# Kernel optimization log

Measured on AMD Instinct MI355X. Metric: run time of the kernel, lower is better.

Reference implementation:

```python
import jax, jax.numpy as jnp
import numpy as np

B, IN_CH, OUT_CH, N_SINCS, COND = 8, 2, 4, 4, 32
K, HOP, T = 256, 64, 65536
FB = K // 2 + 1
EPS = 1e-6


def _windows():
    n = jnp.arange(K, dtype=jnp.float32)
    ola = 0.5 * (1.0 - jnp.cos(2.0 * jnp.pi * n / K))                      # periodic hann
    fir = 0.42 - 0.5 * jnp.cos(2.0 * jnp.pi * n / K) + 0.08 * jnp.cos(4.0 * jnp.pi * n / K)  # periodic blackman
    return ola, fir


def _sinc(x):
    # normalized sinc matching torch.sinc / jnp.sinc, grad-safe near 0
    px = jnp.pi * x
    small = jnp.abs(px) < 1e-4
    px_safe = jnp.where(small, 1.0, px)
    return jnp.where(small, 1.0 - px * px / 6.0, jnp.sin(px_safe) / px_safe)


def _conv1d(x, w, stride, pad):
    return jax.lax.conv_general_dilated(x, w, (stride,), [(pad, pad)],
                                        dimension_numbers=('NCH', 'OIH', 'NCH'))


def setup_inputs() -> dict:
    key = jax.random.key(0)
    ks = jax.random.split(key, 7)
    return {
        'x': jax.random.normal(ks[0], (B, IN_CH, T), jnp.float32),
        'conditioning': jax.random.normal(ks[1], (B, COND, T), jnp.float32),
        'w1': 0.02 * jax.random.normal(ks[2], (COND, COND, K), jnp.float32),
        'b1': 0.01 * jax.random.normal(ks[3], (COND,), jnp.float32),
        'w2': 0.1 * jax.random.normal(ks[4], (IN_CH * OUT_CH * N_SINCS * 2, COND, 1), jnp.float32),
        'b2': 0.01 * jax.random.normal(ks[5], (IN_CH * OUT_CH * N_SINCS * 2,), jnp.float32),
        'bias': jax.random.normal(ks[6], (1, OUT_CH, 1), jnp.float32),
    }


def reference(x, conditioning, w1, b1, w2, b2, bias):
    ola, fir = _windows()

    # ---- filter_net: strided conv -> leaky_relu -> 1x1 conv -> tanh ----
    h = _conv1d(conditioning, w1, HOP, K // 2) + b1[None, :, None]
    h = jnp.where(h >= 0, h, 0.01 * h)
    params = jnp.tanh(_conv1d(h, w2, 1, 0) + b2[None, :, None])   # [B, 2*O*I*S, F]
    nf = params.shape[-1]                                          # = T//HOP + 1 frames

    # channel layout c = ((p*O + o)*I + i)*S + s  ->  [B, O, I, S, F, 2]
    sp = jnp.transpose(params.reshape(B, 2, OUT_CH, IN_CH, N_SINCS, nf), (0, 2, 3, 4, 5, 1))
    amp, width = sp[..., 0], sp[..., 1]                            # [B,O,I,S,F]

    # ---- time-varying sinc FIR synthesis ----
    time_axis = (jnp.linspace(0.0, K - 1, K) - K // 2) / K          # [K]
    sincs = _sinc(width[..., None] * time_axis + EPS) / K           # [B,O,I,S,F,K]
    filt = jnp.einsum('boisf,boisfk->boifk', amp, sincs)           # sum over sincs
    filt = filt * (fir / N_SINCS)                                   # [B,O,I,F,K]
    fft_filt = jnp.swapaxes(jnp.fft.rfft(filt, axis=-1), -1, -2)   # [B,O,I,FB,F] complex

    # ---- STFT (center=True, reflect pad, hann) ----
    xp = jnp.pad(x.reshape(B * IN_CH, T), ((0, 0), (K // 2, K // 2)), mode='reflect')
    idx = jnp.arange(nf)[:, None] * HOP + jnp.arange(K)[None, :]    # [F,K]
    frames = xp[:, idx] * ola                                       # [B*I,F,K]
    X = jnp.swapaxes(jnp.fft.rfft(frames, axis=-1), 1, 2)          # [B*I,FB,F]
    X = X.reshape(B, 1, IN_CH, FB, nf)

    # ---- frequency-domain filtering: complex multiply + reduce over in_channels ----
    Y = (X * fft_filt).sum(2)                                       # [B,O,FB,F]

    # ---- iSTFT (overlap-add, window-square normalization, center trim) ----
    spec = jnp.swapaxes(Y.reshape(B * OUT_CH, FB, nf), 1, 2)        # [B*O,F,FB]
    fr = jnp.fft.irfft(spec, n=K, axis=-1) * ola                    # [B*O,F,K]
    L = HOP * (nf - 1) + K
    y = jnp.zeros((B * OUT_CH, L), jnp.float32).at[:, idx].add(fr)
    env = jnp.zeros((L,), jnp.float32).at[idx].add(jnp.broadcast_to(ola ** 2, (nf, K)))
    y = (y / env)[:, K // 2: K // 2 + HOP * (nf - 1)]               # length T

    return y.reshape(B, OUT_CH, -1) + bias
```

## Files before the change

kernel.cpp:

```cpp
#include <hip/hip_runtime.h>
#include <math.h>

#define NB 8
#define IN_CH 2
#define OUT_CHN 4
#define NSINC 4
#define CONDC 32
#define KK 256
#define HOP 64
#define TT 65536
#define NF 1025
#define LL (HOP*(NF-1)+KK)
#define PI_F 3.14159265358979323846f

#define WTAB_OFF 0
#define PAR_OFF  98304
#define X_OFF    623104
#define ACC_OFF  4821504
#define ACC_N    2105344
#define HPART_OFF 6926848
#define G2_OFF   8042240
#define WFH_OFF  8107776
#define WFL_OFF  8238848

#define FPAD 264

typedef __attribute__((ext_vector_type(8))) short bf16x8;
typedef __attribute__((ext_vector_type(4))) float f32x4;

__device__ __forceinline__ void splitbf(float v, unsigned short& hi, unsigned short& lo) {
    unsigned bits = __float_as_uint(v);
    hi = (unsigned short)(bits >> 16);
    float r = v - __uint_as_float(bits & 0xffff0000u);
    lo = (unsigned short)(__float_as_uint(r) >> 16);
}

__device__ __forceinline__ unsigned short tobf16_rn(float v) {
    unsigned b = __float_as_uint(v);
    return (unsigned short)((b + 0x7FFFu + ((b >> 16) & 1u)) >> 16);
}

__device__ __forceinline__ float frombf16(unsigned short u) {
    return __uint_as_float(((unsigned)u) << 16);
}

__device__ __forceinline__ float sincpoly(float x) {
    float y = PI_F * x;
    float y2 = y * y;
    return 1.f + y2 * (-1.6666667e-1f + y2 * (8.3333333e-3f + y2 * (-1.9841270e-4f
              + y2 * (2.7557319e-6f + y2 * (-2.5052108e-8f)))));
}

__global__ __launch_bounds__(256) void k_setup(unsigned short* __restrict__ wtab,
                                               const float* __restrict__ w1,
                                               unsigned short* __restrict__ wfh,
                                               unsigned short* __restrict__ wfl,
                                               unsigned short* __restrict__ g2u) {
    const int blk = blockIdx.x;
    const int t = threadIdx.x;
    if (blk < 768) {
        int idx = blk * 256 + t;
        int m = idx >> 16;
        int rem = idx & 65535;
        int oc = rem >> 8;
        int kd = rem & 255;
        const float ang = 2.f * PI_F / 256.f;
        float v;
        if (m < 2) {
            if (oc == 0) v = 1.f;
            else if (oc == 1) v = (kd & 1) ? -1.f : 1.f;
            else {
                int nu = oc >> 1;
                float th = ang * (float)((nu * kd) & 255);
                v = (oc & 1) ? -sinf(th) : cosf(th);
            }
            if (m == 0) v *= 0.5f * (1.f - cosf(ang * (float)kd));
        } else {
            float s;
            if (kd == 0) s = 1.f;
            else if (kd == 1) s = (oc & 1) ? -1.f : 1.f;
            else {
                int nu = kd >> 1;
                float th = ang * (float)((nu * oc) & 255);
                s = (kd & 1) ? -2.f * sinf(th) : 2.f * cosf(th);
            }
            v = s * (1.f / 256.f) * 0.5f * (1.f - cosf(ang * (float)oc));
        }
        int nt = oc >> 4, sel = oc & 15;
        int ks = kd >> 5, koct = (kd >> 3) & 3, e = kd & 7;
        wtab[(m << 16) | (nt << 12) | (ks << 9) | (koct << 7) | (sel << 3) | e] = tobf16_rn(v);
    } else if (blk < 1792) {
        int idx = (blk - 768) * 256 + t;
        int c = idx >> 13;
        int cin = (idx >> 8) & 31;
        int k = idx & 255;
        unsigned short hi, lo;
        splitbf(w1[idx], hi, lo);
        int cin2 = cin * 2 + (c >> 4);
        int frag = ((k >> 5) << 9) | (((k >> 3) & 3) << 7) | ((c & 15) << 3) | (k & 7);
        wfh[(cin2 << 12) | frag] = hi;
        wfl[(cin2 << 12) | frag] = lo;
    } else {
        const int wi = blk - 1792;
        const float ang = 2.f * PI_F / 256.f;
        const float w = (float)wi * (1.f / 128.f) - 1.f;
        const int col = t;
        const int nu = col >> 1;
        const float phi = ang * (float)nu;
        const float cphi = cosf(phi), sphi = sinf(phi);
        const float cang = cosf(ang), sang = sinf(ang);
        float c = 1.f, s = 0.f;
        float ca = 1.f, sa = 0.f;
        float sum = 0.f;
        for (int k = 0; k < 256; ++k) {
            float x = w * ((float)k - 128.f) * (1.f / 256.f) + 1e-6f;
            float sp = sincpoly(x);
            float fsc = (0.42f - 0.5f * ca + 0.08f * (2.f * ca * ca - 1.f)) * (1.f / 1024.f);
            float coef;
            if (col == 0) coef = 1.f;
            else if (col == 1) coef = (k & 1) ? -1.f : 1.f;
            else coef = (col & 1) ? -s : c;
            sum += sp * fsc * coef;
            float cn = c * cphi - s * sphi;
            s = s * cphi + c * sphi;
            c = cn;
            float can = ca * cang - sa * sang;
            sa = sa * cang + ca * sang;
            ca = can;
        }
        unsigned short v16 = tobf16_rn(sum);
        if (wi < 256) g2u[2 * ((wi << 8) + col)] = v16;
        if (wi >= 1)  g2u[2 * (((wi - 1) << 8) + col) + 1] = v16;
    }
}

__global__ __launch_bounds__(256) void k_heavy(const float* __restrict__ cond,
                                               const unsigned short* __restrict__ wfh,
                                               const unsigned short* __restrict__ wfl,
                                               float* __restrict__ h_part,
                                               const float* __restrict__ x,
                                               const unsigned short* __restrict__ wtab,
                                               float* __restrict__ X) {
    __shared__ __align__(16) unsigned short s_a[4840];
    const int blk = blockIdx.x;
    const int t = threadIdx.x;
    const int w = t >> 6;
    const int l = t & 63;
    const int sel16 = l & 15;
    const int koct = l >> 4;

    if (blk < 544) {
        const int ftile = blk % 17;
        const int g = (blk / 17) & 3;
        const int b = blk / 68;
        const int f0 = ftile * 64;
        const long pos0 = (long)f0 * HOP - 128;

        const unsigned short* WH = wfh + (l << 3);
        const unsigned short* WL = wfl + (l << 3);

        f32x4 acc0 = {0.f, 0.f, 0.f, 0.f};
        f32x4 acc1 = {0.f, 0.f, 0.f, 0.f};

        for (int ci = 0; ci < 8; ++ci) {
            const int cin = g * 8 + ci;
            __syncthreads();
            const float* crow = &cond[((long)b * CONDC + cin) * TT];
            for (int u = t; u < 4288; u += 256) {
                long p = pos0 + u;
                if (p < 0) p = -p;
                if (p >= TT) p = 2 * (TT - 1) - p;
                int off = u + ((u >> 6) << 3);
                s_a[off] = tobf16_rn(crow[p]);
            }
            __syncthreads();
            const int flocal = w * 16 + sel16;
            const int c20 = (cin * 2) << 12;
            const int c21 = (cin * 2 + 1) << 12;
            #pragma unroll
            for (int ks = 0; ks < 8; ++ks) {
                int u = flocal * 64 + ks * 32 + koct * 8;
                int aoff = u + ((u >> 6) << 3);
                bf16x8 ahi = *(const bf16x8*)&s_a[aoff];
                bf16x8 b0h = *(const bf16x8*)&WH[c20 + (ks << 9)];
                bf16x8 b0l = *(const bf16x8*)&WL[c20 + (ks << 9)];
                bf16x8 b1h = *(const bf16x8*)&WH[c21 + (ks << 9)];
                bf16x8 b1l = *(const bf16x8*)&WL[c21 + (ks << 9)];
                acc0 = __builtin_amdgcn_mfma_f32_16x16x32_bf16(ahi, b0h, acc0, 0, 0, 0);
                acc0 = __builtin_amdgcn_mfma_f32_16x16x32_bf16(ahi, b0l, acc0, 0, 0, 0);
                acc1 = __builtin_amdgcn_mfma_f32_16x16x32_bf16(ahi, b1h, acc1, 0, 0, 0);
                acc1 = __builtin_amdgcn_mfma_f32_16x16x32_bf16(ahi, b1l, acc1, 0, 0, 0);
            }
        }

        #pragma unroll
        for (int j = 0; j < 4; ++j) {
            int f = f0 + w * 16 + koct * 4 + j;
            if (f < NF) {
                long base = (((long)g * NB + b) * NF + f) * CONDC;
                h_part[base + sel16] = acc0[j];
                h_part[base + 16 + sel16] = acc1[j];
            }
        }
    } else {
        const int u2 = blk - 544;
        const int ftile = u2 % 33;
        const int bi = u2 / 33;
        const int f0 = ftile * 32;
        const long pos0 = (long)f0 * HOP - 128;
        const int rh = w & 1;
        const int nh = w >> 1;
        const int flocal = rh * 16 + sel16;

        const float* xrow = &x[(long)bi * TT];
        for (int u = t; u < 2240; u += 256) {
            long p = pos0 + u;
            if (p < 0) p = -p;
            if (p >= TT) p = 2 * (TT - 1) - p;
            int off = u + ((u >> 6) << 3);
            s_a[off] = tobf16_rn(xrow[p]);
        }
        __syncthreads();

        const unsigned short* WF = wtab + (l << 3);
        for (int s = 0; s < 8; ++s) {
            const int nt = nh * 8 + s;
            f32x4 acc = {0.f, 0.f, 0.f, 0.f};
            #pragma unroll
            for (int ks = 0; ks < 8; ++ks) {
                int u = flocal * 64 + ks * 32 + koct * 8;
                int aoff = u + ((u >> 6) << 3);
                bf16x8 ah = *(const bf16x8*)&s_a[aoff];
                bf16x8 bh = *(const bf16x8*)&WF[(nt << 12) + (ks << 9)];
                acc = __builtin_amdgcn_mfma_f32_16x16x32_bf16(ah, bh, acc, 0, 0, 0);
            }
            #pragma unroll
            for (int j = 0; j < 4; ++j) {
                int f = f0 + rh * 16 + koct * 4 + j;
                if (f < NF) X[((long)bi * NF + f) * 256 + nt * 16 + sel16] = acc[j];
            }
        }
    }
}

__global__ __launch_bounds__(64) void k_params(const float* __restrict__ h_part,
                                               const float* __restrict__ w2,
                                               const float* __restrict__ b1,
                                               const float* __restrict__ b2,
                                               float* __restrict__ par,
                                               float* __restrict__ accz) {
    __shared__ float s_h[CONDC];
    const int f = blockIdx.x;
    const int b = blockIdx.y;
    const int t = threadIdx.x;
    {
        int gid = (b * NF + f) * 64 + t;
        for (int u = gid; u < ACC_N; u += NF * NB * 64) accz[u] = 0.f;
    }
    if (t < CONDC) {
        float v = b1[t];
        #pragma unroll
        for (int g = 0; g < 4; ++g)
            v += h_part[(((long)g * NB + b) * NF + f) * CONDC + t];
        s_h[t] = (v >= 0.f) ? v : 0.01f * v;
    }
    __syncthreads();
    float acc = b2[t];
    #pragma unroll 8
    for (int cin = 0; cin < CONDC; ++cin) acc += s_h[cin] * w2[t * CONDC + cin];
    par[((long)b * NF + f) * 64 + t] = tanhf(acc);
}

__global__ __launch_bounds__(256) void k_fused(const float* __restrict__ par,
                                               const unsigned* __restrict__ g2,
                                               const unsigned short* __restrict__ wtab,
                                               const float* __restrict__ X,
                                               float* __restrict__ accb) {
    __shared__ __align__(16) unsigned short s_y[16 * FPAD];
    __shared__ float s_ola[1216];
    __shared__ float s_parl[256];

    const int idx = blockIdx.x;
    const int o = idx / 520;
    const int rem = idx - o * 520;
    const int ftile = rem >> 3;
    const int b = rem & 7;
    const int bo = b * 4 + o;
    const int t = threadIdx.x;
    const int f0 = ftile * 16;
    const int w = t >> 6;
    const int l = t & 63;
    const int sel16 = l & 15;
    const int koct = l >> 4;

    const unsigned short* WI = wtab + 2 * 65536 + (l << 3);

    {
        int f_r = t >> 4;
        int idx2 = t & 15;
        int isel = idx2 >> 3;
        int q = idx2 & 7;
        int col = (o * 2 + isel) * 4 + (q & 3) + ((q >> 2) * 32);
        int fc = f0 + f_r;
        if (fc >= NF) fc = NF - 1;
        s_parl[t] = par[((long)b * NF + fc) * 64 + col];
    }
    __syncthreads();

    #pragma unroll 4
    for (int r = 0; r < 16; ++r) {
        int f = f0 + r;
        bool valid = (f < NF);
        float yv = 0.f;
        #pragma unroll
        for (int i = 0; i < 2; ++i) {
            const float* pp = &s_parl[r * 16 + i * 8];
            float H = 0.f;
            #pragma unroll
            for (int s4 = 0; s4 < 4; ++s4) {
                float a = pp[s4];
                float wv = pp[4 + s4];
                float u = (wv + 1.f) * 128.f;
                float fu = floorf(u);
                int gi = (int)fu;
                gi = (gi < 0) ? 0 : (gi > 255 ? 255 : gi);
                float frac = u - (float)gi;
                unsigned pk = g2[(gi << 8) + t];
                float glo = frombf16((unsigned short)(pk & 0xffffu));
                float ghi = frombf16((unsigned short)(pk >> 16));
                H += a * (glo + frac * (ghi - glo));
            }
            float2 xp = make_float2(0.f, 0.f);
            if (valid) xp = *(const float2*)&X[((long)(b * 2 + i) * NF + f) * 256 + (t & ~1)];
            float Hx = __shfl_xor(H, 1);
            float contrib;
            if (t < 2) contrib = H * ((t & 1) ? xp.y : xp.x);
            else contrib = (t & 1) ? (H * xp.x + Hx * xp.y)
                                   : (H * xp.x - Hx * xp.y);
            yv += contrib;
        }
        s_y[r * FPAD + t] = tobf16_rn(yv);
    }

    __syncthreads();
    for (int u = t; u < 1216; u += 256) s_ola[u] = 0.f;
    __syncthreads();
    for (int s = 0; s < 4; ++s) {
        const int nt = w * 4 + s;
        f32x4 acc = {0.f, 0.f, 0.f, 0.f};
        #pragma unroll
        for (int ks = 0; ks < 8; ++ks) {
            bf16x8 ah = *(const bf16x8*)&s_y[sel16 * FPAD + ks * 32 + koct * 8];
            bf16x8 bh = *(const bf16x8*)&WI[(nt << 12) + (ks << 9)];
            acc = __builtin_amdgcn_mfma_f32_16x16x32_bf16(ah, bh, acc, 0, 0, 0);
        }
        #pragma unroll
        for (int j = 0; j < 4; ++j) {
            int row = koct * 4 + j;
            int n = nt * 16 + sel16;
            atomicAdd(&s_ola[row * 64 + n], acc[j]);
        }
    }
    __syncthreads();
    for (int u = t; u < 1216; u += 256) {
        long pos = (long)f0 * HOP + u;
        if (pos < (long)LL) {
            float v = s_ola[u];
            long base = (long)bo * LL + pos;
            if (u < 192 || u >= 1024) atomicAdd(&accb[base], v);
            else accb[base] = v;
        }
    }
}

__global__ __launch_bounds__(256) void k_norm(const float* __restrict__ accbuf,
                                              const float* __restrict__ bias,
                                              float* __restrict__ out) {
    int idx = blockIdx.x * 256 + threadIdx.x;
    if (idx >= NB * OUT_CHN * TT) return;
    int tpos = idx & (TT - 1);
    int bo = idx >> 16;
    int o = bo & 3;
    int tt = tpos + 128;
    float env;
    if (tt >= 192 && tt < (NF - 1) * HOP) {
        env = 1.5f;
    } else {
        env = 0.f;
        int fhi = tt >> 6;
        #pragma unroll
        for (int d = 0; d < 4; ++d) {
            int f = fhi - d;
            int n = tt - f * HOP;
            if (f >= 0 && f < NF && n >= 0 && n < KK) {
                float angn = (2.f * PI_F / 256.f) * (float)n;
                float wv = 0.5f * (1.f - cosf(angn));
                env += wv * wv;
            }
        }
    }
    out[idx] = accbuf[(long)bo * LL + tt] / env + bias[o];
}

extern "C" void kernel_launch(void* const* d_in, const int* in_sizes, int n_in,
                              void* d_out, int out_size, void* d_ws, size_t ws_size,
                              hipStream_t stream) {
    const float* x    = (const float*)d_in[0];
    const float* cond = (const float*)d_in[1];
    const float* w1   = (const float*)d_in[2];
    const float* b1   = (const float*)d_in[3];
    const float* w2   = (const float*)d_in[4];
    const float* b2   = (const float*)d_in[5];
    const float* bias = (const float*)d_in[6];
    float* out = (float*)d_out;
    float* ws  = (float*)d_ws;
    unsigned short* wtab = (unsigned short*)(ws + WTAB_OFF);
    float* par    = ws + PAR_OFF;
    float* X      = ws + X_OFF;
    float* acc    = ws + ACC_OFF;
    float* h_part = ws + HPART_OFF;
    unsigned* g2  = (unsigned*)(ws + G2_OFF);
    unsigned short* wfh = (unsigned short*)(ws + WFH_OFF);
    unsigned short* wfl = (unsigned short*)(ws + WFL_OFF);

    hipLaunchKernelGGL(k_setup, dim3(2049), dim3(256), 0, stream,
                       wtab, w1, wfh, wfl, (unsigned short*)g2);
    hipLaunchKernelGGL(k_heavy, dim3(1072), dim3(256), 0, stream,
                       cond, wfh, wfl, h_part, x, wtab, X);
    hipLaunchKernelGGL(k_params, dim3(NF, NB), dim3(64), 0, stream, h_part, w2, b1, b2, par, acc);
    hipLaunchKernelGGL(k_fused, dim3(2080), dim3(256), 0, stream, par, g2, wtab, X, acc);
    hipLaunchKernelGGL(k_norm, dim3(8192), dim3(256), 0, stream, acc, bias, out);
}
```

Baseline: 170.1 us.

## Drop bf16 hi/lo split for conv weights and fuse normalization into OLA store

The strided filter-net convolution now uses a single rounded bf16 copy of w1 instead of a hi/lo split pair, which halves the MFMA count and weight loads in that stage. The fused synthesis kernel also writes interior overlap-add samples straight to the output, applying the constant envelope and the bias. k_norm now handles only the boundary regions that still need atomic accumulation. The cost is lower precision in the conditioning convolution and a normalization path that is split across two kernels.

New measurement: 153.6 us, median of 2. 1.11x faster.

```diff
diff --git a/kernel.cpp b/kernel.cpp
--- a/kernel.cpp
+++ b/kernel.cpp
@@ -21,19 +21,11 @@
 #define HPART_OFF 6926848
 #define G2_OFF   8042240
 #define WFH_OFF  8107776
-#define WFL_OFF  8238848
 
 #define FPAD 264
 
 typedef __attribute__((ext_vector_type(8))) short bf16x8;
 typedef __attribute__((ext_vector_type(4))) float f32x4;
-
-__device__ __forceinline__ void splitbf(float v, unsigned short& hi, unsigned short& lo) {
-    unsigned bits = __float_as_uint(v);
-    hi = (unsigned short)(bits >> 16);
-    float r = v - __uint_as_float(bits & 0xffff0000u);
-    lo = (unsigned short)(__float_as_uint(r) >> 16);
-}
 
 __device__ __forceinline__ unsigned short tobf16_rn(float v) {
     unsigned b = __float_as_uint(v);
@@ -54,7 +46,6 @@
 __global__ __launch_bounds__(256) void k_setup(unsigned short* __restrict__ wtab,
                                                const float* __restrict__ w1,
                                                unsigned short* __restrict__ wfh,
-                                               unsigned short* __restrict__ wfl,
                                                unsigned short* __restrict__ g2u) {
     const int blk = blockIdx.x;
     const int t = threadIdx.x;
@@ -94,12 +85,9 @@
         int c = idx >> 13;
         int cin = (idx >> 8) & 31;
         int k = idx & 255;
-        unsigned short hi, lo;
-        splitbf(w1[idx], hi, lo);
         int cin2 = cin * 2 + (c >> 4);
         int frag = ((k >> 5) << 9) | (((k >> 3) & 3) << 7) | ((c & 15) << 3) | (k & 7);
-        wfh[(cin2 << 12) | frag] = hi;
-        wfl[(cin2 << 12) | frag] = lo;
+        wfh[(cin2 << 12) | frag] = tobf16_rn(w1[idx]);
     } else {
         const int wi = blk - 1792;
         const float ang = 2.f * PI_F / 256.f;
@@ -136,7 +124,6 @@
 
 __global__ __launch_bounds__(256) void k_heavy(const float* __restrict__ cond,
                                                const unsigned short* __restrict__ wfh,
-                                               const unsigned short* __restrict__ wfl,
                                                float* __restrict__ h_part,
                                                const float* __restrict__ x,
                                                const unsigned short* __restrict__ wtab,
@@ -157,7 +144,6 @@
         const long pos0 = (long)f0 * HOP - 128;
 
         const unsigned short* WH = wfh + (l << 3);
-        const unsigned short* WL = wfl + (l << 3);
 
         f32x4 acc0 = {0.f, 0.f, 0.f, 0.f};
         f32x4 acc1 = {0.f, 0.f, 0.f, 0.f};
@@ -183,13 +169,9 @@
                 int aoff = u + ((u >> 6) << 3);
                 bf16x8 ahi = *(const bf16x8*)&s_a[aoff];
                 bf16x8 b0h = *(const bf16x8*)&WH[c20 + (ks << 9)];
-                bf16x8 b0l = *(const bf16x8*)&WL[c20 + (ks << 9)];
                 bf16x8 b1h = *(const bf16x8*)&WH[c21 + (ks << 9)];
-                bf16x8 b1l = *(const bf16x8*)&WL[c21 + (ks << 9)];
                 acc0 = __builtin_amdgcn_mfma_f32_16x16x32_bf16(ahi, b0h, acc0, 0, 0, 0);
-                acc0 = __builtin_amdgcn_mfma_f32_16x16x32_bf16(ahi, b0l, acc0, 0, 0, 0);
                 acc1 = __builtin_amdgcn_mfma_f32_16x16x32_bf16(ahi, b1h, acc1, 0, 0, 0);
-                acc1 = __builtin_amdgcn_mfma_f32_16x16x32_bf16(ahi, b1l, acc1, 0, 0, 0);
             }
         }
 
@@ -275,7 +257,9 @@
                                                const unsigned* __restrict__ g2,
                                                const unsigned short* __restrict__ wtab,
                                                const float* __restrict__ X,
-                                               float* __restrict__ accb) {
+                                               float* __restrict__ accb,
+                                               const float* __restrict__ bias,
+                                               float* __restrict__ out) {
     __shared__ __align__(16) unsigned short s_y[16 * FPAD];
     __shared__ float s_ola[1216];
     __shared__ float s_parl[256];
@@ -294,6 +278,7 @@
     const int koct = l >> 4;
 
     const unsigned short* WI = wtab + 2 * 65536 + (l << 3);
+    const float biaso = bias[o];
 
     {
         int f_r = t >> 4;
@@ -364,11 +349,12 @@
     __syncthreads();
     for (int u = t; u < 1216; u += 256) {
         long pos = (long)f0 * HOP + u;
-        if (pos < (long)LL) {
-            float v = s_ola[u];
-            long base = (long)bo * LL + pos;
-            if (u < 192 || u >= 1024) atomicAdd(&accb[base], v);
-            else accb[base] = v;
+        if (pos >= (long)LL) continue;
+        float v = s_ola[u];
+        if (u < 192 || u >= 1024) {
+            atomicAdd(&accb[(long)bo * LL + pos], v);
+        } else if (pos < 65536) {
+            out[(long)bo * TT + (pos - 128)] = v * (1.f / 1.5f) + biaso;
         }
     }
 }
@@ -382,6 +368,7 @@
     int bo = idx >> 16;
     int o = bo & 3;
     int tt = tpos + 128;
+    if (tt >= 192 && tt < 65536 && (tt & 1023) >= 192) return;
     float env;
     if (tt >= 192 && tt < (NF - 1) * HOP) {
         env = 1.5f;
@@ -421,13 +408,12 @@
     float* h_part = ws + HPART_OFF;
     unsigned* g2  = (unsigned*)(ws + G2_OFF);
     unsigned short* wfh = (unsigned short*)(ws + WFH_OFF);
-    unsigned short* wfl = (unsigned short*)(ws + WFL_OFF);
 
     hipLaunchKernelGGL(k_setup, dim3(2049), dim3(256), 0, stream,
-                       wtab, w1, wfh, wfl, (unsigned short*)g2);
+                       wtab, w1, wfh, (unsigned short*)g2);
     hipLaunchKernelGGL(k_heavy, dim3(1072), dim3(256), 0, stream,
-                       cond, wfh, wfl, h_part, x, wtab, X);
+                       cond, wfh, h_part, x, wtab, X);
     hipLaunchKernelGGL(k_params, dim3(NF, NB), dim3(64), 0, stream, h_part, w2, b1, b2, par, acc);
-    hipLaunchKernelGGL(k_fused, dim3(2080), dim3(256), 0, stream, par, g2, wtab, X, acc);
+    hipLaunchKernelGGL(k_fused, dim3(2080), dim3(256), 0, stream, par, g2, wtab, X, acc, bias, out);
     hipLaunchKernelGGL(k_norm, dim3(8192), dim3(256), 0, stream, acc, bias, out);
 }
```
